# Kernel optimization log

Hardware: AMD Instinct MI355X
Metric: run time of the kernel (lower is better)

## Reference

```python
import jax, jax.numpy as jnp
import numpy as np

ATOM_FDIM, BOND_FDIM, HID, DEPTH = 133, 147, 256, 4
N_ATOMS, N_BONDS, MAX_NB, A_PER_MOL = 4096, 8192, 6, 64


def _ln(x, g, b, eps=1e-5):
    mu = x.mean(-1, keepdims=True)
    var = ((x - mu) ** 2).mean(-1, keepdims=True)
    return (x - mu) / jnp.sqrt(var + eps) * g + b


def setup_inputs() -> dict:
    key = jax.random.key(0)
    ks = jax.random.split(key, 20)
    def w(k, i, o):
        return jax.random.normal(k, (i, o), jnp.float32) / np.sqrt(i).astype(np.float32)
    return {
        "f_atoms": jax.random.normal(ks[0], (N_ATOMS, ATOM_FDIM), jnp.float32),
        "f_bonds": jax.random.normal(ks[1], (N_BONDS, BOND_FDIM), jnp.float32),
        "Wq_atom": w(ks[2], ATOM_FDIM, ATOM_FDIM),
        "Wk_atom": w(ks[3], ATOM_FDIM, ATOM_FDIM),
        "Wv_atom": w(ks[4], ATOM_FDIM, ATOM_FDIM),
        "ln_g": jnp.ones((ATOM_FDIM,), jnp.float32),
        "ln_b": jnp.zeros((ATOM_FDIM,), jnp.float32),
        "Wi": w(ks[5], BOND_FDIM, HID),
        "Wh": w(ks[6], HID, HID),
        "Wq": w(ks[7], HID, HID),
        "Wk": w(ks[8], HID, HID),
        "Wv": w(ks[9], HID, HID),
        "Wa": w(ks[10], HID, HID),
        "Walpha_w": w(ks[11], 2 * HID, 1),
        "Walpha_b": jnp.zeros((1,), jnp.float32),
        "Wo_w": w(ks[12], ATOM_FDIM + HID, HID),
        "Wo_b": jnp.zeros((HID,), jnp.float32),
        "Wb_w": w(ks[13], HID, HID),
        "Wb_b": jnp.zeros((HID,), jnp.float32),
        "a2b": jax.random.randint(ks[14], (N_ATOMS, MAX_NB), 0, N_BONDS),
        "b2a": jax.random.randint(ks[15], (N_BONDS,), 0, N_ATOMS),
        "b2revb": jax.random.randint(ks[16], (N_BONDS,), 0, N_BONDS),
        "atoms_per_mol": A_PER_MOL,
    }


def reference(f_atoms, f_bonds, Wq_atom, Wk_atom, Wv_atom, ln_g, ln_b, Wi, Wh,
              Wq, Wk, Wv, Wa, Walpha_w, Walpha_b, Wo_w, Wo_b, Wb_w, Wb_b,
              a2b, b2a, b2revb, atoms_per_mol):
    M = f_atoms.shape[0] // atoms_per_mol
    fdim = f_atoms.shape[1]
    # --- per-molecule atom self-attention enhancement (uniform a_scope) ---
    x = f_atoms.reshape(M, atoms_per_mol, fdim)  # [M, A, F]
    q, k, v = x @ Wq_atom, x @ Wk_atom, x @ Wv_atom
    scores = jnp.einsum('maf,mbf->mab', q, k) / np.sqrt(fdim).astype(np.float32)
    attn_out = jnp.einsum('mab,mbf->maf', jax.nn.softmax(scores, -1), v)
    f_atoms_e = _ln(x + attn_out, ln_g, ln_b).reshape(-1, fdim)

    # --- bond message init ---
    inputs = f_bonds @ Wi                      # [B, H]
    message = jax.nn.relu(inputs)
    sqrt_h = np.sqrt(HID).astype(np.float32)

    for _ in range(DEPTH - 1):
        # DMPNN gather-sum
        a_message = message[a2b].sum(1)        # [N_atoms, H]
        dmpnn = (a_message[b2a] - message[b2revb]) @ Wh
        # global bond-bond attention (faithful to torch: over all messages)
        Q, K, V = message @ Wq, message @ Wk, message @ Wv
        att_w = jax.nn.softmax(Q @ K.T / sqrt_h, -1)   # [B, B]
        att_msg = (att_w @ V) @ Wa
        alpha = jax.nn.sigmoid(
            jnp.concatenate([dmpnn, att_msg], -1) @ Walpha_w + Walpha_b)
        message = jax.nn.relu(inputs + alpha * dmpnn + (1.0 - alpha) * att_msg)
        # dropout is identity in eval mode

    # --- atom readout ---
    a_message = message[a2b].sum(1)
    a_input = jnp.concatenate([f_atoms_e, a_message], 1)
    atom_h = jax.nn.relu(a_input @ Wo_w + Wo_b)        # [N_atoms, H]

    # --- per-molecule attentive pooling ---
    hm = atom_h.reshape(M, atoms_per_mol, HID)
    aw = jax.nn.softmax(jnp.einsum('mah,mbh->mab', hm @ Wa, hm), -1)
    att_h = jax.nn.relu(jnp.einsum('mab,mbh->mah', aw, hm) @ Wb_w + Wb_b)
    mol_vecs = (hm + att_h).sum(1) / atoms_per_mol
    return mol_vecs
```

## Files before the change

kernel.cpp:

```cpp
#include <hip/hip_runtime.h>
#include <hip/hip_bf16.h>

typedef __hip_bfloat16 hbf16;
typedef __bf16 bf16x8 __attribute__((ext_vector_type(8)));
typedef float floatx4 __attribute__((ext_vector_type(4)));

#define N_ATOMS 4096
#define N_BONDS 8192
#define FDIM 133
#define BFDIM 147
#define HID 256
#define APM 64
#define NMOL 64
#define FA_S 160
#define FB_S 160
#define AI_S 416
#define CS 8

struct P8 { float* p[8]; };
struct QKV { const hbf16* w[3]; hbf16* outp[3]; };
struct CvtTab { const void* src[6]; float* dst[6]; int n[6]; };
struct WTab { const void* src[11]; hbf16* dst[11]; int K[11]; int Hout[11]; int Kp[11]; int total[11]; };

__device__ __forceinline__ float bcvt(hbf16 x) { return __bfloat162float(x); }

__device__ __forceinline__ float load_in(const void* src, int i, int f32flag)
{
    return f32flag ? ((const float*)src)[i] : bcvt(((const hbf16*)src)[i]);
}

__device__ __forceinline__ void split8(const float4 a0, const float4 a1,
                                       bf16x8& hi, bf16x8& lo)
{
    const float v[8] = {a0.x, a0.y, a0.z, a0.w, a1.x, a1.y, a1.z, a1.w};
    #pragma unroll
    for (int i = 0; i < 8; i++) {
        const __bf16 h = (__bf16)v[i];
        hi[i] = h;
        lo[i] = (__bf16)(v[i] - (float)h);
    }
}

__global__ void detect_kernel(const unsigned short* __restrict__ probe, int* __restrict__ flag)
{
    const int t = threadIdx.x;
    float mx = 0.f;
    for (int i = t; i < 4096; i += 64) {
        unsigned int u = ((unsigned int)probe[i]) << 16;
        float v;
        __builtin_memcpy(&v, &u, 4);
        v = fabsf(v);
        if (!(v == v)) v = 0.f;
        if (v > 1e6f) v = 1e6f;
        mx = fmaxf(mx, v);
    }
    #pragma unroll
    for (int o = 32; o > 0; o >>= 1) mx = fmaxf(mx, __shfl_xor(mx, o));
    if (t == 0) *flag = (mx > 100.f) ? 1 : 0;
}

__global__ void small_cvt_kernel(CvtTab tab, const int* __restrict__ flag)
{
    const int f32 = *flag;
    for (int s = 0; s < 6; s++)
        for (int i = threadIdx.x; i < tab.n[s]; i += 256)
            tab.dst[s][i] = load_in(tab.src[s], i, f32);
}

__global__ void cvt_pad_kernel(const void* __restrict__ src, float* __restrict__ dst,
                               int N, int K, int Kp, const int* __restrict__ flag)
{
    const int i = blockIdx.x * 256 + threadIdx.x;
    if (i >= N * Kp) return;
    const int r = i / Kp, k = i - r * Kp;
    dst[i] = (k < K) ? load_in(src, r * K + k, *flag) : 0.f;
}

__global__ void wt_all_kernel(WTab tab, const int* __restrict__ flag)
{
    const int wid = blockIdx.y;
    const int f32 = *flag;
    const int tot = tab.total[wid], Kp = tab.Kp[wid], K = tab.K[wid], Hout = tab.Hout[wid];
    hbf16* dst = tab.dst[wid];
    const void* src = tab.src[wid];
    for (int i = blockIdx.x * 256 + threadIdx.x; i < tot; i += gridDim.x * 256) {
        const int n = i / Kp, k = i - n * Kp;
        const float v = (k < K && n < Hout) ? load_in(src, k * Hout + n, f32) : 0.f;
        dst[i] = __float2bfloat16(v);
    }
}

__global__ __launch_bounds__(256)
void mgemm_kernel(const float* __restrict__ A, int lda, const hbf16* __restrict__ Wt,
                  const float* __restrict__ bias,
                  float* __restrict__ Cf, float* __restrict__ Cf2, int ldcf,
                  hbf16* __restrict__ Cbh, hbf16* __restrict__ Cbl, int ldcb,
                  hbf16* __restrict__ CbT, int ldct,
                  int Hout, int HoutStore, int relu)
{
    const int t = threadIdx.x, w = t >> 6, ln = t & 63;
    const int lane16 = ln & 15, quad = ln >> 4;
    const int rb = blockIdx.y * 64 + w * 16, cb = blockIdx.x * 64;
    const floatx4 zero4 = {0.f, 0.f, 0.f, 0.f};
    floatx4 acc[4] = {zero4, zero4, zero4, zero4};
    const float* ar = A + (size_t)(rb + lane16) * lda + quad * 8;
    for (int kk = 0; kk < lda; kk += 32) {
        const float4 a0 = *(const float4*)(ar + kk);
        const float4 a1 = *(const float4*)(ar + kk + 4);
        bf16x8 af;
        af[0] = (__bf16)a0.x; af[1] = (__bf16)a0.y; af[2] = (__bf16)a0.z; af[3] = (__bf16)a0.w;
        af[4] = (__bf16)a1.x; af[5] = (__bf16)a1.y; af[6] = (__bf16)a1.z; af[7] = (__bf16)a1.w;
        #pragma unroll
        for (int nt = 0; nt < 4; nt++) {
            const bf16x8 bf =
                *(const bf16x8*)&Wt[(size_t)(cb + nt * 16 + lane16) * lda + kk + quad * 8];
            acc[nt] = __builtin_amdgcn_mfma_f32_16x16x32_bf16(af, bf, acc[nt], 0, 0, 0);
        }
    }
    #pragma unroll
    for (int nt = 0; nt < 4; nt++) {
        const int n = cb + nt * 16 + lane16;
        if (n >= HoutStore) continue;
        const bool valid = n < Hout;
        const float bv = (bias && valid) ? bias[n] : 0.f;
        #pragma unroll
        for (int r = 0; r < 4; r++) {
            const int m = rb + quad * 4 + r;
            float v = valid ? acc[nt][r] + bv : 0.f;
            if (relu) v = fmaxf(v, 0.f);
            if (Cf)  Cf[(size_t)m * ldcf + n] = v;
            if (Cf2) Cf2[(size_t)m * ldcf + n] = fmaxf(v, 0.f);
            if (Cbh) {
                const hbf16 h = __float2bfloat16(v);
                Cbh[(size_t)m * ldcb + n] = h;
                if (Cbl) Cbl[(size_t)m * ldcb + n] = __float2bfloat16(v - bcvt(h));
            }
            if (CbT) CbT[(size_t)n * ldct + m] = __float2bfloat16(v);
        }
    }
}

__global__ __launch_bounds__(256)
void qkv_kernel(const float* __restrict__ A, QKV q)
{
    const int z = blockIdx.z;
    const hbf16* __restrict__ Wt = q.w[z];
    hbf16* __restrict__ outp = q.outp[z];
    const int t = threadIdx.x, w = t >> 6, ln = t & 63;
    const int lane16 = ln & 15, quad = ln >> 4;
    const int rb = blockIdx.y * 64 + w * 16, cb = blockIdx.x * 64;
    const floatx4 zero4 = {0.f, 0.f, 0.f, 0.f};
    floatx4 acc[4] = {zero4, zero4, zero4, zero4};
    const float* ar = A + (size_t)(rb + lane16) * HID + quad * 8;
    for (int kk = 0; kk < HID; kk += 32) {
        const float4 a0 = *(const float4*)(ar + kk);
        const float4 a1 = *(const float4*)(ar + kk + 4);
        bf16x8 af;
        af[0] = (__bf16)a0.x; af[1] = (__bf16)a0.y; af[2] = (__bf16)a0.z; af[3] = (__bf16)a0.w;
        af[4] = (__bf16)a1.x; af[5] = (__bf16)a1.y; af[6] = (__bf16)a1.z; af[7] = (__bf16)a1.w;
        #pragma unroll
        for (int nt = 0; nt < 4; nt++) {
            const bf16x8 bf =
                *(const bf16x8*)&Wt[(size_t)(cb + nt * 16 + lane16) * HID + kk + quad * 8];
            acc[nt] = __builtin_amdgcn_mfma_f32_16x16x32_bf16(af, bf, acc[nt], 0, 0, 0);
        }
    }
    #pragma unroll
    for (int nt = 0; nt < 4; nt++) {
        const int n = cb + nt * 16 + lane16;
        #pragma unroll
        for (int r = 0; r < 4; r++) {
            const int m = rb + quad * 4 + r;
            const hbf16 h = __float2bfloat16(acc[nt][r]);
            if (z < 2) outp[(size_t)m * HID + n] = h;
            else       outp[(size_t)n * N_BONDS + m] = h;
        }
    }
}

__global__ __launch_bounds__(256)
void atom_fused_kernel(const float* __restrict__ qa, const float* __restrict__ ka,
                       const hbf16* __restrict__ vT, const float* __restrict__ f_atoms_p,
                       const float* __restrict__ ln_g, const float* __restrict__ ln_b,
                       float* __restrict__ f_e)
{
    __shared__ float S[64][68];
    __shared__ __bf16 P[64][72];
    __shared__ float Y[64][136];
    const int m = blockIdx.x, t = threadIdx.x;
    const int w = t >> 6, ln = t & 63;
    const int lane16 = ln & 15, quad = ln >> 4;
    const int base = m * APM;
    const floatx4 zero4 = {0.f, 0.f, 0.f, 0.f};

    {
        floatx4 acc[4] = {zero4, zero4, zero4, zero4};
        const float* arow = qa + (size_t)(base + w * 16 + lane16) * FA_S + quad * 8;
        #pragma unroll
        for (int ks = 0; ks < 5; ks++) {
            bf16x8 ah, al;
            split8(*(const float4*)(arow + ks * 32), *(const float4*)(arow + ks * 32 + 4), ah, al);
            #pragma unroll
            for (int nt = 0; nt < 4; nt++) {
                const float* brow = ka + (size_t)(base + nt * 16 + lane16) * FA_S + ks * 32 + quad * 8;
                bf16x8 bh, bl;
                split8(*(const float4*)brow, *(const float4*)(brow + 4), bh, bl);
                acc[nt] = __builtin_amdgcn_mfma_f32_16x16x32_bf16(ah, bh, acc[nt], 0, 0, 0);
                acc[nt] = __builtin_amdgcn_mfma_f32_16x16x32_bf16(al, bh, acc[nt], 0, 0, 0);
                acc[nt] = __builtin_amdgcn_mfma_f32_16x16x32_bf16(ah, bl, acc[nt], 0, 0, 0);
            }
        }
        const float scale = 1.f / sqrtf(133.f);
        #pragma unroll
        for (int nt = 0; nt < 4; nt++)
            #pragma unroll
            for (int r = 0; r < 4; r++)
                S[w * 16 + quad * 4 + r][nt * 16 + lane16] = acc[nt][r] * scale;
    }
    for (int r = w * 16; r < w * 16 + 16; r++) {
        const float x = S[r][ln];
        float mx = x;
        #pragma unroll
        for (int o = 32; o > 0; o >>= 1) mx = fmaxf(mx, __shfl_xor(mx, o));
        const float p = __expf(x - mx);
        float sm = p;
        #pragma unroll
        for (int o = 32; o > 0; o >>= 1) sm += __shfl_xor(sm, o);
        P[r][ln] = (__bf16)(p / sm);
    }
    {
        floatx4 o[9];
        #pragma unroll
        for (int i = 0; i < 9; i++) o[i] = zero4;
        #pragma unroll
        for (int ks = 0; ks < 2; ks++) {
            const bf16x8 af = *(const bf16x8*)&P[w * 16 + lane16][ks * 32 + quad * 8];
            #pragma unroll
            for (int nt = 0; nt < 9; nt++) {
                const bf16x8 bfv =
                    *(const bf16x8*)&vT[(size_t)(nt * 16 + lane16) * N_ATOMS + base + ks * 32 + quad * 8];
                o[nt] = __builtin_amdgcn_mfma_f32_16x16x32_bf16(af, bfv, o[nt], 0, 0, 0);
            }
        }
        #pragma unroll
        for (int nt = 0; nt < 9; nt++) {
            const int f = nt * 16 + lane16;
            if (f >= FDIM) continue;
            #pragma unroll
            for (int r = 0; r < 4; r++) {
                const int a = w * 16 + quad * 4 + r;
                Y[a][f] = f_atoms_p[(size_t)(base + a) * FA_S + f] + o[nt][r];
            }
        }
    }
    for (int r = w * 16; r < w * 16 + 16; r++) {
        float sum = 0.f, sq = 0.f;
        for (int f = ln; f < FDIM; f += 64) { const float v = Y[r][f]; sum += v; sq += v * v; }
        #pragma unroll
        for (int o = 32; o > 0; o >>= 1) { sum += __shfl_xor(sum, o); sq += __shfl_xor(sq, o); }
        const float mu = sum / FDIM;
        const float var = sq / FDIM - mu * mu;
        const float rstd = rsqrtf(var + 1e-5f);
        for (int f = ln; f < FDIM; f += 64) {
            const float v = (Y[r][f] - mu) * rstd;
            f_e[(size_t)(base + r) * FDIM + f] = v * ln_g[f] + ln_b[f];
        }
    }
}

__global__ __launch_bounds__(256)
void pool_fused_kernel(const float* __restrict__ hmWa, const float* __restrict__ atom_h,
                       const hbf16* __restrict__ hm_hi, const hbf16* __restrict__ hm_lo,
                       const hbf16* __restrict__ hmT, const hbf16* __restrict__ Wtb,
                       const float* __restrict__ Wb_b, void* __restrict__ out,
                       const int* __restrict__ flag)
{
    __shared__ float S[64][68];
    __shared__ __bf16 P[64][72];
    __shared__ __bf16 att[64][264];
    const int m = blockIdx.x, t = threadIdx.x;
    const int w = t >> 6, ln = t & 63;
    const int lane16 = ln & 15, quad = ln >> 4;
    const int base = m * APM;
    const floatx4 zero4 = {0.f, 0.f, 0.f, 0.f};

    {
        floatx4 acc[4] = {zero4, zero4, zero4, zero4};
        const float* arow = hmWa + (size_t)(base + w * 16 + lane16) * HID + quad * 8;
        #pragma unroll
        for (int ks = 0; ks < 8; ks++) {
            bf16x8 ah, al;
            split8(*(const float4*)(arow + ks * 32), *(const float4*)(arow + ks * 32 + 4), ah, al);
            #pragma unroll
            for (int nt = 0; nt < 4; nt++) {
                const size_t bidx = (size_t)(base + nt * 16 + lane16) * HID + ks * 32 + quad * 8;
                const bf16x8 bh = *(const bf16x8*)&hm_hi[bidx];
                const bf16x8 bl = *(const bf16x8*)&hm_lo[bidx];
                acc[nt] = __builtin_amdgcn_mfma_f32_16x16x32_bf16(ah, bh, acc[nt], 0, 0, 0);
                acc[nt] = __builtin_amdgcn_mfma_f32_16x16x32_bf16(al, bh, acc[nt], 0, 0, 0);
                acc[nt] = __builtin_amdgcn_mfma_f32_16x16x32_bf16(ah, bl, acc[nt], 0, 0, 0);
            }
        }
        #pragma unroll
        for (int nt = 0; nt < 4; nt++)
            #pragma unroll
            for (int r = 0; r < 4; r++)
                S[w * 16 + quad * 4 + r][nt * 16 + lane16] = acc[nt][r];
    }
    for (int r = w * 16; r < w * 16 + 16; r++) {
        const float x = S[r][ln];
        float mx = x;
        #pragma unroll
        for (int o = 32; o > 0; o >>= 1) mx = fmaxf(mx, __shfl_xor(mx, o));
        const float p = __expf(x - mx);
        float sm = p;
        #pragma unroll
        for (int o = 32; o > 0; o >>= 1) sm += __shfl_xor(sm, o);
        P[r][ln] = (__bf16)(p / sm);
    }
    __syncthreads();
    {
        floatx4 o3[4][4];
        #pragma unroll
        for (int mt = 0; mt < 4; mt++)
            #pragma unroll
            for (int nt = 0; nt < 4; nt++) o3[mt][nt] = zero4;
        #pragma unroll
        for (int ks = 0; ks < 2; ks++) {
            bf16x8 af[4];
            #pragma unroll
            for (int mt = 0; mt < 4; mt++)
                af[mt] = *(const bf16x8*)&P[mt * 16 + lane16][ks * 32 + quad * 8];
            #pragma unroll
            for (int nt = 0; nt < 4; nt++) {
                const bf16x8 bfv = *(const bf16x8*)
                    &hmT[(size_t)(w * 64 + nt * 16 + lane16) * N_ATOMS + base + ks * 32 + quad * 8];
                #pragma unroll
                for (int mt = 0; mt < 4; mt++)
                    o3[mt][nt] = __builtin_amdgcn_mfma_f32_16x16x32_bf16(af[mt], bfv, o3[mt][nt], 0, 0, 0);
            }
        }
        #pragma unroll
        for (int mt = 0; mt < 4; mt++)
            #pragma unroll
            for (int nt = 0; nt < 4; nt++)
                #pragma unroll
                for (int r = 0; r < 4; r++)
                    att[mt * 16 + quad * 4 + r][w * 64 + nt * 16 + lane16] = (__bf16)o3[mt][nt][r];
    }
    __syncthreads();
    {
        floatx4 o5[4][4];
        #pragma unroll
        for (int mt = 0; mt < 4; mt++)
            #pragma unroll
            for (int nt = 0; nt < 4; nt++) o5[mt][nt] = zero4;
        #pragma unroll
        for (int ks = 0; ks < 8; ks++) {
            bf16x8 af[4];
            #pragma unroll
            for (int mt = 0; mt < 4; mt++)
                af[mt] = *(const bf16x8*)&att[mt * 16 + lane16][ks * 32 + quad * 8];
            #pragma unroll
            for (int nt = 0; nt < 4; nt++) {
                const bf16x8 bfv = *(const bf16x8*)
                    &Wtb[(size_t)(w * 64 + nt * 16 + lane16) * HID + ks * 32 + quad * 8];
                #pragma unroll
                for (int mt = 0; mt < 4; mt++)
                    o5[mt][nt] = __builtin_amdgcn_mfma_f32_16x16x32_bf16(af[mt], bfv, o5[mt][nt], 0, 0, 0);
            }
        }
        #pragma unroll
        for (int nt = 0; nt < 4; nt++) {
            const int n = w * 64 + nt * 16 + lane16;
            const float bv = Wb_b[n];
            float s = 0.f;
            #pragma unroll
            for (int mt = 0; mt < 4; mt++)
                #pragma unroll
                for (int r = 0; r < 4; r++)
                    s += fmaxf(o5[mt][nt][r] + bv, 0.f);
            s += __shfl_xor(s, 16);
            s += __shfl_xor(s, 32);
            if (quad == 0) {
                float hsum = 0.f;
                for (int a = 0; a < APM; a++)
                    hsum += atom_h[(size_t)(base + a) * HID + n];
                const float v = (s + hsum) * (1.f / 64.f);
                if (*flag) ((float*)out)[m * HID + n] = v;
                else       ((hbf16*)out)[m * HID + n] = __float2bfloat16(v);
            }
        }
    }
}

__global__ __launch_bounds__(256, 2)
void flash_kernel(const hbf16* __restrict__ Qg, const hbf16* __restrict__ Kg,
                  const hbf16* __restrict__ Vtg, P8 parts, float2* __restrict__ ml)
{
    __shared__ __align__(16) __bf16 Ks[32][256];
    __shared__ __align__(16) __bf16 Vt[256][32];
    __shared__ __align__(16) __bf16 Ps[4][16][40];

    const int t = threadIdx.x, w = t >> 6, ln = t & 63;
    const int lane16 = ln & 15, quad = ln >> 4;
    const int cs = blockIdx.x;
    const int rw = blockIdx.y * 64 + w * 16;
    float* __restrict__ part = parts.p[cs];

    bf16x8 qf[8];
    #pragma unroll
    for (int ks = 0; ks < 8; ks++)
        qf[ks] = *(const bf16x8*)&Qg[(size_t)(rw + lane16) * HID + ks * 32 + quad * 8];

    const floatx4 zero4 = {0.f, 0.f, 0.f, 0.f};
    floatx4 O[16];
    #pragma unroll
    for (int i = 0; i < 16; i++) O[i] = zero4;
    float mrow[4] = {-1e30f, -1e30f, -1e30f, -1e30f};
    float lrow[4] = {0.f, 0.f, 0.f, 0.f};
    const float scale = 0.0625f;

    const int cbeg = cs * (N_BONDS / CS), cend = cbeg + N_BONDS / CS;
    for (int c0 = cbeg; c0 < cend; c0 += 32) {
        __syncthreads();
        #pragma unroll
        for (int ii = 0; ii < 4; ii++) {
            const int idx = t + ii * 256;
            const int row = idx >> 5, c = idx & 31;
            *(bf16x8*)&Ks[row][(c ^ (row & 31)) * 8] =
                *(const bf16x8*)&Kg[(size_t)(c0 + row) * HID + c * 8];
        }
        #pragma unroll
        for (int ii = 0; ii < 4; ii++) {
            const int idx = t + ii * 256;
            const int row = idx >> 2, c = idx & 3;
            *(bf16x8*)&Vt[row][(c ^ (row & 3)) * 8] =
                *(const bf16x8*)&Vtg[(size_t)row * N_BONDS + c0 + c * 8];
        }
        __syncthreads();

        floatx4 s0 = zero4, s1 = zero4;
        #pragma unroll
        for (int ks = 0; ks < 8; ks++) {
            const int ch = ks * 4 + quad;
            const bf16x8 b0 = *(bf16x8*)&Ks[lane16][(ch ^ lane16) * 8];
            const bf16x8 b1 = *(bf16x8*)&Ks[16 + lane16][(ch ^ (16 + lane16)) * 8];
            s0 = __builtin_amdgcn_mfma_f32_16x16x32_bf16(qf[ks], b0, s0, 0, 0, 0);
            s1 = __builtin_amdgcn_mfma_f32_16x16x32_bf16(qf[ks], b1, s1, 0, 0, 0);
        }
        float alpha[4];
        #pragma unroll
        for (int r = 0; r < 4; r++) {
            const float v0 = s0[r] * scale, v1 = s1[r] * scale;
            float mx = fmaxf(v0, v1);
            #pragma unroll
            for (int o = 8; o > 0; o >>= 1) mx = fmaxf(mx, __shfl_xor(mx, o));
            const float mnew = fmaxf(mrow[r], mx);
            const float p0 = __expf(v0 - mnew), p1 = __expf(v1 - mnew);
            float ps = p0 + p1;
            #pragma unroll
            for (int o = 8; o > 0; o >>= 1) ps += __shfl_xor(ps, o);
            alpha[r] = __expf(mrow[r] - mnew);
            lrow[r] = lrow[r] * alpha[r] + ps;
            mrow[r] = mnew;
            const int row = quad * 4 + r;
            Ps[w][row][lane16] = (__bf16)p0;
            Ps[w][row][16 + lane16] = (__bf16)p1;
        }
        const bool need = (alpha[0] < 1.f) | (alpha[1] < 1.f) | (alpha[2] < 1.f) | (alpha[3] < 1.f);
        if (__any(need)) {
            #pragma unroll
            for (int nt = 0; nt < 16; nt++)
                #pragma unroll
                for (int r = 0; r < 4; r++) O[nt][r] *= alpha[r];
        }
        const bf16x8 pf = *(bf16x8*)&Ps[w][lane16][quad * 8];
        #pragma unroll
        for (int nt = 0; nt < 16; nt++) {
            const int vrow = nt * 16 + lane16;
            const bf16x8 vf = *(bf16x8*)&Vt[vrow][(quad ^ (vrow & 3)) * 8];
            O[nt] = __builtin_amdgcn_mfma_f32_16x16x32_bf16(pf, vf, O[nt], 0, 0, 0);
        }
    }
    #pragma unroll
    for (int r = 0; r < 4; r++) {
        const int row = rw + quad * 4 + r;
        #pragma unroll
        for (int nt = 0; nt < 16; nt++)
            part[(size_t)row * HID + nt * 16 + lane16] = O[nt][r];
        if (lane16 == 0) ml[cs * N_BONDS + row] = make_float2(mrow[r], lrow[r]);
    }
}

__global__ void flash_combine_kernel(P8 parts, const float2* __restrict__ ml,
                                     float* __restrict__ out)
{
    const int row = blockIdx.x, h = threadIdx.x;
    float2 e[CS];
    float M = -1e30f;
    #pragma unroll
    for (int i = 0; i < CS; i++) { e[i] = ml[i * N_BONDS + row]; M = fmaxf(M, e[i].x); }
    float den = 0.f, val = 0.f;
    #pragma unroll
    for (int i = 0; i < CS; i++) {
        const float wgt = __expf(e[i].x - M);
        den += wgt * e[i].y;
        val += wgt * parts.p[i][(size_t)row * HID + h];
    }
    out[(size_t)row * HID + h] = val / den;
}

__global__ void gather_kernel(const float* __restrict__ msg, const int* __restrict__ a2b,
                              float* __restrict__ amsg)
{
    const int a = blockIdx.x, h = threadIdx.x;
    float s = 0.f;
    #pragma unroll
    for (int i = 0; i < 6; i++) {
        const int b = a2b[a * 6 + i];
        s += msg[(size_t)b * HID + h];
    }
    amsg[(size_t)a * HID + h] = s;
}

__global__ void pre_kernel(const float* __restrict__ amsg, const float* __restrict__ msg,
                           const int* __restrict__ b2a, const int* __restrict__ b2revb,
                           float* __restrict__ pre)
{
    const int b = blockIdx.x, h = threadIdx.x;
    pre[(size_t)b * HID + h] =
        amsg[(size_t)b2a[b] * HID + h] - msg[(size_t)b2revb[b] * HID + h];
}

__global__ __launch_bounds__(256)
void combine_kernel(const float* __restrict__ inputs, const float* __restrict__ dmpnn,
                    const float* __restrict__ att, const float* __restrict__ ww,
                    const float* __restrict__ wb, float* __restrict__ msg)
{
    const int wv = threadIdx.x >> 6, lnid = threadIdx.x & 63;
    const int row = blockIdx.x * 4 + wv;
    const float* dr = dmpnn + (size_t)row * HID;
    const float* ar = att + (size_t)row * HID;
    float dot = 0.f;
    for (int h = lnid; h < HID; h += 64)
        dot += dr[h] * ww[h] + ar[h] * ww[HID + h];
    #pragma unroll
    for (int o = 32; o > 0; o >>= 1) dot += __shfl_xor(dot, o);
    const float alpha = 1.f / (1.f + __expf(-(dot + wb[0])));
    for (int h = lnid; h < HID; h += 64) {
        const float v = inputs[(size_t)row * HID + h] + alpha * dr[h] + (1.f - alpha) * ar[h];
        msg[(size_t)row * HID + h] = fmaxf(v, 0.f);
    }
}

__global__ void concat_kernel(const float* __restrict__ fe, const float* __restrict__ amsg,
                              float* __restrict__ ai)
{
    const int a = blockIdx.x, t = threadIdx.x;
    for (int f = t; f < FDIM; f += 256) ai[(size_t)a * AI_S + f] = fe[(size_t)a * FDIM + f];
    for (int h = t; h < HID; h += 256) ai[(size_t)a * AI_S + FDIM + h] = amsg[(size_t)a * HID + h];
    for (int z = t; z < AI_S - FDIM - HID; z += 256) ai[(size_t)a * AI_S + FDIM + HID + z] = 0.f;
}

extern "C" void kernel_launch(void* const* d_in, const int* in_sizes, int n_in,
                              void* d_out, int out_size, void* d_ws, size_t ws_size,
                              hipStream_t stream)
{
    const int* a2b    = (const int*)d_in[19];
    const int* b2a    = (const int*)d_in[20];
    const int* b2revb = (const int*)d_in[21];

    float* ws = (float*)d_ws;
    size_t off = 0;
    auto alloc = [&](size_t n) { float* p = ws + off; off += (n + 63) & ~(size_t)63; return p; };
    int* flag = (int*)alloc(64);

    float* ln_g     = alloc(FDIM);
    float* ln_b     = alloc(FDIM);
    float* Walpha_w = alloc(2 * HID);
    float* Walpha_b = alloc(64);
    float* Wo_b     = alloc(HID);
    float* Wb_b     = alloc(HID);
    float* f_atoms_p = alloc((size_t)N_ATOMS * FA_S);
    float* f_bonds_p = alloc((size_t)N_BONDS * FB_S);
    auto balloc = [&](size_t n) { return (hbf16*)alloc((n + 1) / 2); };
    hbf16* Wt_qa = balloc((size_t)192 * FA_S);
    hbf16* Wt_ka = balloc((size_t)192 * FA_S);
    hbf16* Wt_va = balloc((size_t)192 * FA_S);
    hbf16* Wt_i  = balloc((size_t)HID * FB_S);
    hbf16* Wt_h  = balloc((size_t)HID * HID);
    hbf16* Wt_q  = balloc((size_t)HID * HID);
    hbf16* Wt_k  = balloc((size_t)HID * HID);
    hbf16* Wt_v  = balloc((size_t)HID * HID);
    hbf16* Wt_a  = balloc((size_t)HID * HID);
    hbf16* Wt_b  = balloc((size_t)HID * HID);
    hbf16* Wt_o  = balloc((size_t)HID * AI_S);

    float* f_e    = alloc((size_t)N_ATOMS * FDIM);
    float* inputs = alloc((size_t)N_BONDS * HID);
    float* msg    = alloc((size_t)N_BONDS * HID);
    float* buf1   = alloc((size_t)N_BONDS * HID);
    float* buf2   = alloc((size_t)N_BONDS * HID);
    float* buf3   = alloc((size_t)N_BONDS * HID);
    float* buf4   = alloc((size_t)N_BONDS * HID);
    float* pnew   = alloc((size_t)N_BONDS * HID);
    float* pext0  = alloc((size_t)N_BONDS * HID);
    float* pext1  = alloc((size_t)N_BONDS * HID);
    float* pext2  = alloc((size_t)N_BONDS * HID);
    float* pext3  = alloc((size_t)N_BONDS * HID);
    float* amsg   = alloc((size_t)N_ATOMS * HID);
    float2* ml    = (float2*)alloc((size_t)CS * N_BONDS * 2);
    hbf16* Qb  = balloc((size_t)N_BONDS * HID);
    hbf16* Kb  = balloc((size_t)N_BONDS * HID);
    hbf16* Vtg = balloc((size_t)N_BONDS * HID);
    hbf16* vTa = (hbf16*)buf3;

    detect_kernel<<<1, 64, 0, stream>>>((const unsigned short*)d_in[1], flag);

    CvtTab ct;
    ct.src[0] = d_in[5];  ct.dst[0] = ln_g;     ct.n[0] = FDIM;
    ct.src[1] = d_in[6];  ct.dst[1] = ln_b;     ct.n[1] = FDIM;
    ct.src[2] = d_in[13]; ct.dst[2] = Walpha_w; ct.n[2] = 2 * HID;
    ct.src[3] = d_in[14]; ct.dst[3] = Walpha_b; ct.n[3] = 1;
    ct.src[4] = d_in[16]; ct.dst[4] = Wo_b;     ct.n[4] = HID;
    ct.src[5] = d_in[18]; ct.dst[5] = Wb_b;     ct.n[5] = HID;
    small_cvt_kernel<<<1, 256, 0, stream>>>(ct, flag);

    cvt_pad_kernel<<<(N_ATOMS * FA_S + 255) / 256, 256, 0, stream>>>(
        d_in[0], f_atoms_p, N_ATOMS, FDIM, FA_S, flag);
    cvt_pad_kernel<<<(N_BONDS * FB_S + 255) / 256, 256, 0, stream>>>(
        d_in[1], f_bonds_p, N_BONDS, BFDIM, FB_S, flag);

    WTab wt;
    const void* wsrc[11] = {d_in[2], d_in[3], d_in[4], d_in[7], d_in[8], d_in[9],
                            d_in[10], d_in[11], d_in[12], d_in[17], d_in[15]};
    hbf16* wdst[11] = {Wt_qa, Wt_ka, Wt_va, Wt_i, Wt_h, Wt_q, Wt_k, Wt_v, Wt_a, Wt_b, Wt_o};
    const int wK[11]  = {FDIM, FDIM, FDIM, BFDIM, HID, HID, HID, HID, HID, HID, FDIM + HID};
    const int wH[11]  = {FDIM, FDIM, FDIM, HID, HID, HID, HID, HID, HID, HID, HID};
    const int wKp[11] = {FA_S, FA_S, FA_S, FB_S, HID, HID, HID, HID, HID, HID, AI_S};
    const int wHp[11] = {192, 192, 192, HID, HID, HID, HID, HID, HID, HID, HID};
    for (int i = 0; i < 11; i++) {
        wt.src[i] = wsrc[i]; wt.dst[i] = wdst[i]; wt.K[i] = wK[i]; wt.Hout[i] = wH[i];
        wt.Kp[i] = wKp[i]; wt.total[i] = wHp[i] * wKp[i];
    }
    wt_all_kernel<<<dim3(416, 11), 256, 0, stream>>>(wt, flag);

    auto mg = [&](const float* A, int lda, const hbf16* Wt, const float* bias,
                  float* Cf, float* Cf2, int ldcf, hbf16* Cbh, hbf16* Cbl, int ldcb,
                  hbf16* CbT, int ldct, int rows, int Hout, int HoutStore, int relu) {
        dim3 grid((HoutStore + 63) / 64, rows / 64);
        mgemm_kernel<<<grid, 256, 0, stream>>>(A, lda, Wt, bias, Cf, Cf2, ldcf,
                                               Cbh, Cbl, ldcb, CbT, ldct,
                                               Hout, HoutStore, relu);
    };

    mg(f_atoms_p, FA_S, Wt_qa, nullptr, buf1, nullptr, FA_S, nullptr, nullptr, 0,
       nullptr, 0, N_ATOMS, FDIM, FA_S, 0);
    mg(f_atoms_p, FA_S, Wt_ka, nullptr, buf2, nullptr, FA_S, nullptr, nullptr, 0,
       nullptr, 0, N_ATOMS, FDIM, FA_S, 0);
    mg(f_atoms_p, FA_S, Wt_va, nullptr, nullptr, nullptr, 0, nullptr, nullptr, 0,
       vTa, N_ATOMS, N_ATOMS, FDIM, 192, 0);
    atom_fused_kernel<<<NMOL, 256, 0, stream>>>(buf1, buf2, vTa, f_atoms_p, ln_g, ln_b, f_e);

    mg(f_bonds_p, FB_S, Wt_i, nullptr, inputs, msg, HID, nullptr, nullptr, 0,
       nullptr, 0, N_BONDS, HID, HID, 0);

    P8 parts;
    parts.p[0] = buf1; parts.p[1] = buf3; parts.p[2] = buf4; parts.p[3] = pnew;
    parts.p[4] = pext0; parts.p[5] = pext1; parts.p[6] = pext2; parts.p[7] = pext3;
    QKV qkv;
    qkv.w[0] = Wt_q; qkv.w[1] = Wt_k; qkv.w[2] = Wt_v;
    qkv.outp[0] = Qb; qkv.outp[1] = Kb; qkv.outp[2] = Vtg;

    for (int d = 0; d < 3; d++) {
        gather_kernel<<<N_ATOMS, 256, 0, stream>>>(msg, a2b, amsg);
        pre_kernel<<<N_BONDS, 256, 0, stream>>>(amsg, msg, b2a, b2revb, buf1);
        mg(buf1, HID, Wt_h, nullptr, buf2, nullptr, HID, nullptr, nullptr, 0,
           nullptr, 0, N_BONDS, HID, HID, 0);
        qkv_kernel<<<dim3(4, N_BONDS / 64, 3), 256, 0, stream>>>(msg, qkv);
        flash_kernel<<<dim3(CS, N_BONDS / 64), 256, 0, stream>>>(Qb, Kb, Vtg, parts, ml);
        flash_combine_kernel<<<N_BONDS, 256, 0, stream>>>(parts, ml, buf3);
        mg(buf3, HID, Wt_a, nullptr, buf4, nullptr, HID, nullptr, nullptr, 0,
           nullptr, 0, N_BONDS, HID, HID, 0);
        combine_kernel<<<N_BONDS / 4, 256, 0, stream>>>(inputs, buf2, buf4, Walpha_w,
                                                        Walpha_b, msg);
    }

    gather_kernel<<<N_ATOMS, 256, 0, stream>>>(msg, a2b, amsg);
    concat_kernel<<<N_ATOMS, 256, 0, stream>>>(f_e, amsg, buf1);
    mg(buf1, AI_S, Wt_o, Wo_b, buf4, nullptr, HID, Qb, Kb, HID,
       Vtg, N_ATOMS, N_ATOMS, HID, HID, 1);

    mg(buf4, HID, Wt_a, nullptr, buf3, nullptr, HID, nullptr, nullptr, 0,
       nullptr, 0, N_ATOMS, HID, HID, 0);
    pool_fused_kernel<<<NMOL, 256, 0, stream>>>(buf3, buf4, Qb, Kb, Vtg, Wt_b,
                                                Wb_b, d_out, flag);
}
```

Baseline: 1.061 ms.

## Fuse flash split combine with Wa GEMM and gating; double rows per flash wave

Each flash-attention wave now processes 32 query rows instead of 16, so every K/V tile loaded into shared memory feeds twice as many MFMAs. The split-KV combine, the Wa projection and the alpha-gated relu update are merged into one kernel that rebuilds the attention output in LDS as bf16 and writes msg directly. The atom gather and the bond pre-subtraction are also merged into a single kernel. This removes several launches and intermediate global round trips, at the cost of higher register pressure in the flash kernel, half as many flash blocks, and a bf16 rounding of the attention output before Wa.

```diff
diff --git a/kernel.cpp b/kernel.cpp
--- a/kernel.cpp
+++ b/kernel.cpp
@@ -400,25 +400,32 @@
 {
     __shared__ __align__(16) __bf16 Ks[32][256];
     __shared__ __align__(16) __bf16 Vt[256][32];
-    __shared__ __align__(16) __bf16 Ps[4][16][40];
+    __shared__ __align__(16) __bf16 Ps[4][32][40];
 
     const int t = threadIdx.x, w = t >> 6, ln = t & 63;
     const int lane16 = ln & 15, quad = ln >> 4;
     const int cs = blockIdx.x;
-    const int rw = blockIdx.y * 64 + w * 16;
+    const int rw = blockIdx.y * 128 + w * 32;
     float* __restrict__ part = parts.p[cs];
 
-    bf16x8 qf[8];
-    #pragma unroll
-    for (int ks = 0; ks < 8; ks++)
-        qf[ks] = *(const bf16x8*)&Qg[(size_t)(rw + lane16) * HID + ks * 32 + quad * 8];
+    bf16x8 qf[2][8];
+    #pragma unroll
+    for (int mt = 0; mt < 2; mt++)
+        #pragma unroll
+        for (int ks = 0; ks < 8; ks++)
+            qf[mt][ks] = *(const bf16x8*)&Qg[(size_t)(rw + mt * 16 + lane16) * HID + ks * 32 + quad * 8];
 
     const floatx4 zero4 = {0.f, 0.f, 0.f, 0.f};
-    floatx4 O[16];
-    #pragma unroll
-    for (int i = 0; i < 16; i++) O[i] = zero4;
-    float mrow[4] = {-1e30f, -1e30f, -1e30f, -1e30f};
-    float lrow[4] = {0.f, 0.f, 0.f, 0.f};
+    floatx4 O[2][16];
+    #pragma unroll
+    for (int mt = 0; mt < 2; mt++)
+        #pragma unroll
+        for (int i = 0; i < 16; i++) O[mt][i] = zero4;
+    float mrow[2][4], lrow[2][4];
+    #pragma unroll
+    for (int mt = 0; mt < 2; mt++)
+        #pragma unroll
+        for (int r = 0; r < 4; r++) { mrow[mt][r] = -1e30f; lrow[mt][r] = 0.f; }
     const float scale = 0.0625f;
 
     const int cbeg = cs * (N_BONDS / CS), cend = cbeg + N_BONDS / CS;
@@ -440,75 +447,157 @@
         }
         __syncthreads();
 
-        floatx4 s0 = zero4, s1 = zero4;
+        floatx4 s[2][2] = {{zero4, zero4}, {zero4, zero4}};
         #pragma unroll
         for (int ks = 0; ks < 8; ks++) {
             const int ch = ks * 4 + quad;
             const bf16x8 b0 = *(bf16x8*)&Ks[lane16][(ch ^ lane16) * 8];
             const bf16x8 b1 = *(bf16x8*)&Ks[16 + lane16][(ch ^ (16 + lane16)) * 8];
-            s0 = __builtin_amdgcn_mfma_f32_16x16x32_bf16(qf[ks], b0, s0, 0, 0, 0);
-            s1 = __builtin_amdgcn_mfma_f32_16x16x32_bf16(qf[ks], b1, s1, 0, 0, 0);
-        }
-        float alpha[4];
-        #pragma unroll
-        for (int r = 0; r < 4; r++) {
-            const float v0 = s0[r] * scale, v1 = s1[r] * scale;
-            float mx = fmaxf(v0, v1);
-            #pragma unroll
-            for (int o = 8; o > 0; o >>= 1) mx = fmaxf(mx, __shfl_xor(mx, o));
-            const float mnew = fmaxf(mrow[r], mx);
-            const float p0 = __expf(v0 - mnew), p1 = __expf(v1 - mnew);
-            float ps = p0 + p1;
-            #pragma unroll
-            for (int o = 8; o > 0; o >>= 1) ps += __shfl_xor(ps, o);
-            alpha[r] = __expf(mrow[r] - mnew);
-            lrow[r] = lrow[r] * alpha[r] + ps;
-            mrow[r] = mnew;
-            const int row = quad * 4 + r;
-            Ps[w][row][lane16] = (__bf16)p0;
-            Ps[w][row][16 + lane16] = (__bf16)p1;
-        }
-        const bool need = (alpha[0] < 1.f) | (alpha[1] < 1.f) | (alpha[2] < 1.f) | (alpha[3] < 1.f);
+            #pragma unroll
+            for (int mt = 0; mt < 2; mt++) {
+                s[mt][0] = __builtin_amdgcn_mfma_f32_16x16x32_bf16(qf[mt][ks], b0, s[mt][0], 0, 0, 0);
+                s[mt][1] = __builtin_amdgcn_mfma_f32_16x16x32_bf16(qf[mt][ks], b1, s[mt][1], 0, 0, 0);
+            }
+        }
+        float alpha[2][4];
+        bool need = false;
+        #pragma unroll
+        for (int mt = 0; mt < 2; mt++)
+            #pragma unroll
+            for (int r = 0; r < 4; r++) {
+                const float v0 = s[mt][0][r] * scale, v1 = s[mt][1][r] * scale;
+                float mx = fmaxf(v0, v1);
+                #pragma unroll
+                for (int o = 8; o > 0; o >>= 1) mx = fmaxf(mx, __shfl_xor(mx, o));
+                const float mnew = fmaxf(mrow[mt][r], mx);
+                const float p0 = __expf(v0 - mnew), p1 = __expf(v1 - mnew);
+                float ps = p0 + p1;
+                #pragma unroll
+                for (int o = 8; o > 0; o >>= 1) ps += __shfl_xor(ps, o);
+                alpha[mt][r] = __expf(mrow[mt][r] - mnew);
+                need |= (alpha[mt][r] < 1.f);
+                lrow[mt][r] = lrow[mt][r] * alpha[mt][r] + ps;
+                mrow[mt][r] = mnew;
+                const int row = mt * 16 + quad * 4 + r;
+                Ps[w][row][lane16] = (__bf16)p0;
+                Ps[w][row][16 + lane16] = (__bf16)p1;
+            }
         if (__any(need)) {
             #pragma unroll
-            for (int nt = 0; nt < 16; nt++)
+            for (int mt = 0; mt < 2; mt++)
                 #pragma unroll
-                for (int r = 0; r < 4; r++) O[nt][r] *= alpha[r];
-        }
-        const bf16x8 pf = *(bf16x8*)&Ps[w][lane16][quad * 8];
+                for (int nt = 0; nt < 16; nt++)
+                    #pragma unroll
+                    for (int r = 0; r < 4; r++) O[mt][nt][r] *= alpha[mt][r];
+        }
+        bf16x8 pf[2];
+        #pragma unroll
+        for (int mt = 0; mt < 2; mt++)
+            pf[mt] = *(bf16x8*)&Ps[w][mt * 16 + lane16][quad * 8];
         #pragma unroll
         for (int nt = 0; nt < 16; nt++) {
             const int vrow = nt * 16 + lane16;
             const bf16x8 vf = *(bf16x8*)&Vt[vrow][(quad ^ (vrow & 3)) * 8];
-            O[nt] = __builtin_amdgcn_mfma_f32_16x16x32_bf16(pf, vf, O[nt], 0, 0, 0);
-        }
-    }
+            #pragma unroll
+            for (int mt = 0; mt < 2; mt++)
+                O[mt][nt] = __builtin_amdgcn_mfma_f32_16x16x32_bf16(pf[mt], vf, O[mt][nt], 0, 0, 0);
+        }
+    }
+    #pragma unroll
+    for (int mt = 0; mt < 2; mt++)
+        #pragma unroll
+        for (int r = 0; r < 4; r++) {
+            const int row = rw + mt * 16 + quad * 4 + r;
+            #pragma unroll
+            for (int nt = 0; nt < 16; nt++)
+                part[(size_t)row * HID + nt * 16 + lane16] = O[mt][nt][r];
+            if (lane16 == 0) ml[cs * N_BONDS + row] = make_float2(mrow[mt][r], lrow[mt][r]);
+        }
+}
+
+__global__ __launch_bounds__(256)
+void attcombine_kernel(P8 parts, const float2* __restrict__ ml, const hbf16* __restrict__ Wta,
+                       const float* __restrict__ inputs, const float* __restrict__ dmpnn,
+                       const float* __restrict__ ww, const float* __restrict__ wb,
+                       float* __restrict__ msg)
+{
+    __shared__ __align__(16) __bf16 Av[64][264];
+    __shared__ float wgtS[64][10];
+    const int t = threadIdx.x, w = t >> 6, ln = t & 63;
+    const int lane16 = ln & 15, quad = ln >> 4;
+    const int rb = blockIdx.x * 64;
+
+    if (t < 64) {
+        const int row = rb + t;
+        float2 e[CS];
+        float M = -1e30f;
+        #pragma unroll
+        for (int i = 0; i < CS; i++) { e[i] = ml[i * N_BONDS + row]; M = fmaxf(M, e[i].x); }
+        float den = 0.f;
+        #pragma unroll
+        for (int i = 0; i < CS; i++) {
+            const float g = __expf(e[i].x - M);
+            wgtS[t][i] = g;
+            den += g * e[i].y;
+        }
+        wgtS[t][8] = 1.f / den;
+    }
+    __syncthreads();
+    for (int e = t; e < 64 * 64; e += 256) {
+        const int row = e >> 6, c4 = (e & 63) * 4;
+        const float inv = wgtS[row][8];
+        float ax = 0.f, ay = 0.f, az = 0.f, aw = 0.f;
+        #pragma unroll
+        for (int i = 0; i < CS; i++) {
+            const float g = wgtS[row][i];
+            const float4 pv = *(const float4*)&parts.p[i][(size_t)(rb + row) * HID + c4];
+            ax += g * pv.x; ay += g * pv.y; az += g * pv.z; aw += g * pv.w;
+        }
+        Av[row][c4 + 0] = (__bf16)(ax * inv);
+        Av[row][c4 + 1] = (__bf16)(ay * inv);
+        Av[row][c4 + 2] = (__bf16)(az * inv);
+        Av[row][c4 + 3] = (__bf16)(aw * inv);
+    }
+    __syncthreads();
+
+    const floatx4 zero4 = {0.f, 0.f, 0.f, 0.f};
+    floatx4 acc[16];
+    #pragma unroll
+    for (int nt = 0; nt < 16; nt++) acc[nt] = zero4;
+    #pragma unroll
+    for (int ks = 0; ks < 8; ks++) {
+        const bf16x8 af = *(const bf16x8*)&Av[w * 16 + lane16][ks * 32 + quad * 8];
+        #pragma unroll
+        for (int nt = 0; nt < 16; nt++) {
+            const bf16x8 bf = *(const bf16x8*)&Wta[(size_t)(nt * 16 + lane16) * HID + ks * 32 + quad * 8];
+            acc[nt] = __builtin_amdgcn_mfma_f32_16x16x32_bf16(af, bf, acc[nt], 0, 0, 0);
+        }
+    }
+    float w2[16];
+    #pragma unroll
+    for (int nt = 0; nt < 16; nt++) w2[nt] = ww[HID + nt * 16 + lane16];
     #pragma unroll
     for (int r = 0; r < 4; r++) {
-        const int row = rw + quad * 4 + r;
-        #pragma unroll
-        for (int nt = 0; nt < 16; nt++)
-            part[(size_t)row * HID + nt * 16 + lane16] = O[nt][r];
-        if (lane16 == 0) ml[cs * N_BONDS + row] = make_float2(mrow[r], lrow[r]);
-    }
-}
-
-__global__ void flash_combine_kernel(P8 parts, const float2* __restrict__ ml,
-                                     float* __restrict__ out)
-{
-    const int row = blockIdx.x, h = threadIdx.x;
-    float2 e[CS];
-    float M = -1e30f;
-    #pragma unroll
-    for (int i = 0; i < CS; i++) { e[i] = ml[i * N_BONDS + row]; M = fmaxf(M, e[i].x); }
-    float den = 0.f, val = 0.f;
-    #pragma unroll
-    for (int i = 0; i < CS; i++) {
-        const float wgt = __expf(e[i].x - M);
-        den += wgt * e[i].y;
-        val += wgt * parts.p[i][(size_t)row * HID + h];
-    }
-    out[(size_t)row * HID + h] = val / den;
+        const int row = rb + w * 16 + quad * 4 + r;
+        float dv[16], iv[16];
+        float dot = 0.f;
+        #pragma unroll
+        for (int nt = 0; nt < 16; nt++) {
+            const int col = nt * 16 + lane16;
+            dv[nt] = dmpnn[(size_t)row * HID + col];
+            iv[nt] = inputs[(size_t)row * HID + col];
+            dot += acc[nt][r] * w2[nt] + dv[nt] * ww[col];
+        }
+        #pragma unroll
+        for (int o = 8; o > 0; o >>= 1) dot += __shfl_xor(dot, o);
+        const float alpha = 1.f / (1.f + __expf(-(dot + wb[0])));
+        #pragma unroll
+        for (int nt = 0; nt < 16; nt++) {
+            const int col = nt * 16 + lane16;
+            const float v = iv[nt] + alpha * dv[nt] + (1.f - alpha) * acc[nt][r];
+            msg[(size_t)row * HID + col] = fmaxf(v, 0.f);
+        }
+    }
 }
 
 __global__ void gather_kernel(const float* __restrict__ msg, const int* __restrict__ a2b,
@@ -524,34 +613,17 @@
     amsg[(size_t)a * HID + h] = s;
 }
 
-__global__ void pre_kernel(const float* __restrict__ amsg, const float* __restrict__ msg,
-                           const int* __restrict__ b2a, const int* __restrict__ b2revb,
-                           float* __restrict__ pre)
+__global__ void gather_pre_kernel(const float* __restrict__ msg, const int* __restrict__ a2b,
+                                  const int* __restrict__ b2a, const int* __restrict__ b2revb,
+                                  float* __restrict__ pre)
 {
     const int b = blockIdx.x, h = threadIdx.x;
-    pre[(size_t)b * HID + h] =
-        amsg[(size_t)b2a[b] * HID + h] - msg[(size_t)b2revb[b] * HID + h];
-}
-
-__global__ __launch_bounds__(256)
-void combine_kernel(const float* __restrict__ inputs, const float* __restrict__ dmpnn,
-                    const float* __restrict__ att, const float* __restrict__ ww,
-                    const float* __restrict__ wb, float* __restrict__ msg)
-{
-    const int wv = threadIdx.x >> 6, lnid = threadIdx.x & 63;
-    const int row = blockIdx.x * 4 + wv;
-    const float* dr = dmpnn + (size_t)row * HID;
-    const float* ar = att + (size_t)row * HID;
-    float dot = 0.f;
-    for (int h = lnid; h < HID; h += 64)
-        dot += dr[h] * ww[h] + ar[h] * ww[HID + h];
-    #pragma unroll
-    for (int o = 32; o > 0; o >>= 1) dot += __shfl_xor(dot, o);
-    const float alpha = 1.f / (1.f + __expf(-(dot + wb[0])));
-    for (int h = lnid; h < HID; h += 64) {
-        const float v = inputs[(size_t)row * HID + h] + alpha * dr[h] + (1.f - alpha) * ar[h];
-        msg[(size_t)row * HID + h] = fmaxf(v, 0.f);
-    }
+    const int a = b2a[b];
+    float s = -msg[(size_t)b2revb[b] * HID + h];
+    #pragma unroll
+    for (int i = 0; i < 6; i++)
+        s += msg[(size_t)a2b[a * 6 + i] * HID + h];
+    pre[(size_t)b * HID + h] = s;
 }
 
 __global__ void concat_kernel(const float* __restrict__ fe, const float* __restrict__ amsg,
@@ -674,17 +746,13 @@
     qkv.outp[0] = Qb; qkv.outp[1] = Kb; qkv.outp[2] = Vtg;
 
     for (int d = 0; d < 3; d++) {
-        gather_kernel<<<N_ATOMS, 256, 0, stream>>>(msg, a2b, amsg);
-        pre_kernel<<<N_BONDS, 256, 0, stream>>>(amsg, msg, b2a, b2revb, buf1);
+        gather_pre_kernel<<<N_BONDS, 256, 0, stream>>>(msg, a2b, b2a, b2revb, buf1);
         mg(buf1, HID, Wt_h, nullptr, buf2, nullptr, HID, nullptr, nullptr, 0,
            nullptr, 0, N_BONDS, HID, HID, 0);
         qkv_kernel<<<dim3(4, N_BONDS / 64, 3), 256, 0, stream>>>(msg, qkv);
-        flash_kernel<<<dim3(CS, N_BONDS / 64), 256, 0, stream>>>(Qb, Kb, Vtg, parts, ml);
-        flash_combine_kernel<<<N_BONDS, 256, 0, stream>>>(parts, ml, buf3);
-        mg(buf3, HID, Wt_a, nullptr, buf4, nullptr, HID, nullptr, nullptr, 0,
-           nullptr, 0, N_BONDS, HID, HID, 0);
-        combine_kernel<<<N_BONDS / 4, 256, 0, stream>>>(inputs, buf2, buf4, Walpha_w,
-                                                        Walpha_b, msg);
+        flash_kernel<<<dim3(CS, N_BONDS / 128), 256, 0, stream>>>(Qb, Kb, Vtg, parts, ml);
+        attcombine_kernel<<<N_BONDS / 64, 256, 0, stream>>>(parts, ml, Wt_a, inputs,
+                                                            buf2, Walpha_w, Walpha_b, msg);
     }
 
     gather_kernel<<<N_ATOMS, 256, 0, stream>>>(msg, a2b, amsg);
```

Result: slower. 1.236 ms (+16.5%).

## Fuse depth-loop kernels: gather+pre, Wh into QKV launch, flash-combine+Wa+gating

Applied to the files above, without the earlier changes.

Merges the atom gather and bond pre-subtraction into one kernel and folds the Wh projection into the batched Q/K/V projection launch. The flash partial combine, Wa projection, alpha gate and ReLU update now run in a single kernel per 32-row tile. This cuts launches and round trips of intermediate bond-sized buffers through global memory. It also changes the flash kernel occupancy hint to 3 waves per EU. The Wh and Wa projections now use single bf16 inputs instead of the previous generic GEMM path, which may reduce accuracy.

```diff
diff --git a/kernel.cpp b/kernel.cpp
--- a/kernel.cpp
+++ b/kernel.cpp
@@ -18,7 +18,7 @@
 #define CS 8
 
 struct P8 { float* p[8]; };
-struct QKV { const hbf16* w[3]; hbf16* outp[3]; };
+struct PROJ { const float* A[4]; const hbf16* w[4]; void* outp[4]; int mode[4]; };
 struct CvtTab { const void* src[6]; float* dst[6]; int n[6]; };
 struct WTab { const void* src[11]; hbf16* dst[11]; int K[11]; int Hout[11]; int Kp[11]; int total[11]; };
 
@@ -141,11 +141,13 @@
 }
 
 __global__ __launch_bounds__(256)
-void qkv_kernel(const float* __restrict__ A, QKV q)
+void proj_kernel(PROJ p)
 {
     const int z = blockIdx.z;
-    const hbf16* __restrict__ Wt = q.w[z];
-    hbf16* __restrict__ outp = q.outp[z];
+    const float* __restrict__ A = p.A[z];
+    const hbf16* __restrict__ Wt = p.w[z];
+    void* __restrict__ outp = p.outp[z];
+    const int mode = p.mode[z];
     const int t = threadIdx.x, w = t >> 6, ln = t & 63;
     const int lane16 = ln & 15, quad = ln >> 4;
     const int rb = blockIdx.y * 64 + w * 16, cb = blockIdx.x * 64;
@@ -171,9 +173,10 @@
         #pragma unroll
         for (int r = 0; r < 4; r++) {
             const int m = rb + quad * 4 + r;
-            const hbf16 h = __float2bfloat16(acc[nt][r]);
-            if (z < 2) outp[(size_t)m * HID + n] = h;
-            else       outp[(size_t)n * N_BONDS + m] = h;
+            const float v = acc[nt][r];
+            if (mode == 2)      ((float*)outp)[(size_t)m * HID + n] = v;
+            else if (mode == 0) ((hbf16*)outp)[(size_t)m * HID + n] = __float2bfloat16(v);
+            else                ((hbf16*)outp)[(size_t)n * N_BONDS + m] = __float2bfloat16(v);
         }
     }
 }
@@ -394,7 +397,7 @@
     }
 }
 
-__global__ __launch_bounds__(256, 2)
+__global__ __launch_bounds__(256) __attribute__((amdgpu_waves_per_eu(3, 3)))
 void flash_kernel(const hbf16* __restrict__ Qg, const hbf16* __restrict__ Kg,
                   const hbf16* __restrict__ Vtg, P8 parts, float2* __restrict__ ml)
 {
@@ -493,22 +496,96 @@
     }
 }
 
-__global__ void flash_combine_kernel(P8 parts, const float2* __restrict__ ml,
-                                     float* __restrict__ out)
-{
-    const int row = blockIdx.x, h = threadIdx.x;
-    float2 e[CS];
-    float M = -1e30f;
-    #pragma unroll
-    for (int i = 0; i < CS; i++) { e[i] = ml[i * N_BONDS + row]; M = fmaxf(M, e[i].x); }
-    float den = 0.f, val = 0.f;
-    #pragma unroll
-    for (int i = 0; i < CS; i++) {
-        const float wgt = __expf(e[i].x - M);
-        den += wgt * e[i].y;
-        val += wgt * parts.p[i][(size_t)row * HID + h];
-    }
-    out[(size_t)row * HID + h] = val / den;
+__global__ __launch_bounds__(256)
+void attcombine_kernel(P8 parts, const float2* __restrict__ ml, const hbf16* __restrict__ Wta,
+                       const float* __restrict__ inputs, const float* __restrict__ dmpnn,
+                       const float* __restrict__ ww, const float* __restrict__ wb,
+                       float* __restrict__ msg)
+{
+    __shared__ __align__(16) __bf16 Av[32][264];
+    __shared__ float wgtS[32][10];
+    __shared__ float dotS[32][2];
+    const int t = threadIdx.x, w = t >> 6, ln = t & 63;
+    const int lane16 = ln & 15, quad = ln >> 4;
+    const int rb = blockIdx.x * 32;
+    const int mt = w & 1, nh = w >> 1;
+
+    if (t < 32) {
+        const int row = rb + t;
+        float2 e[CS];
+        float M = -1e30f;
+        #pragma unroll
+        for (int i = 0; i < CS; i++) { e[i] = ml[i * N_BONDS + row]; M = fmaxf(M, e[i].x); }
+        float den = 0.f;
+        #pragma unroll
+        for (int i = 0; i < CS; i++) {
+            const float g = __expf(e[i].x - M);
+            wgtS[t][i] = g;
+            den += g * e[i].y;
+        }
+        wgtS[t][8] = 1.f / den;
+    }
+    __syncthreads();
+    for (int e = t; e < 32 * 64; e += 256) {
+        const int row = e >> 6, c4 = (e & 63) * 4;
+        const float inv = wgtS[row][8];
+        float ax = 0.f, ay = 0.f, az = 0.f, aw = 0.f;
+        #pragma unroll
+        for (int i = 0; i < CS; i++) {
+            const float g = wgtS[row][i];
+            const float4 pv = *(const float4*)&parts.p[i][(size_t)(rb + row) * HID + c4];
+            ax += g * pv.x; ay += g * pv.y; az += g * pv.z; aw += g * pv.w;
+        }
+        Av[row][c4 + 0] = (__bf16)(ax * inv);
+        Av[row][c4 + 1] = (__bf16)(ay * inv);
+        Av[row][c4 + 2] = (__bf16)(az * inv);
+        Av[row][c4 + 3] = (__bf16)(aw * inv);
+    }
+    __syncthreads();
+
+    const floatx4 zero4 = {0.f, 0.f, 0.f, 0.f};
+    floatx4 acc[8];
+    #pragma unroll
+    for (int nt = 0; nt < 8; nt++) acc[nt] = zero4;
+    #pragma unroll
+    for (int ks = 0; ks < 8; ks++) {
+        const bf16x8 af = *(const bf16x8*)&Av[mt * 16 + lane16][ks * 32 + quad * 8];
+        #pragma unroll
+        for (int nt = 0; nt < 8; nt++) {
+            const bf16x8 bf = *(const bf16x8*)
+                &Wta[(size_t)(nh * 128 + nt * 16 + lane16) * HID + ks * 32 + quad * 8];
+            acc[nt] = __builtin_amdgcn_mfma_f32_16x16x32_bf16(af, bf, acc[nt], 0, 0, 0);
+        }
+    }
+    float w2[8];
+    #pragma unroll
+    for (int nt = 0; nt < 8; nt++) w2[nt] = ww[HID + nh * 128 + nt * 16 + lane16];
+    #pragma unroll
+    for (int r = 0; r < 4; r++) {
+        const int row = rb + mt * 16 + quad * 4 + r;
+        float dot = 0.f;
+        #pragma unroll
+        for (int nt = 0; nt < 8; nt++) {
+            const int col = nh * 128 + nt * 16 + lane16;
+            dot += acc[nt][r] * w2[nt] + dmpnn[(size_t)row * HID + col] * ww[col];
+        }
+        #pragma unroll
+        for (int o = 8; o > 0; o >>= 1) dot += __shfl_xor(dot, o);
+        if (lane16 == 0) dotS[row - rb][nh] = dot;
+    }
+    __syncthreads();
+    #pragma unroll
+    for (int r = 0; r < 4; r++) {
+        const int row = rb + mt * 16 + quad * 4 + r;
+        const float alpha = 1.f / (1.f + __expf(-(dotS[row - rb][0] + dotS[row - rb][1] + wb[0])));
+        #pragma unroll
+        for (int nt = 0; nt < 8; nt++) {
+            const int col = nh * 128 + nt * 16 + lane16;
+            const float dv = dmpnn[(size_t)row * HID + col];
+            const float v = inputs[(size_t)row * HID + col] + alpha * dv + (1.f - alpha) * acc[nt][r];
+            msg[(size_t)row * HID + col] = fmaxf(v, 0.f);
+        }
+    }
 }
 
 __global__ void gather_kernel(const float* __restrict__ msg, const int* __restrict__ a2b,
@@ -524,34 +601,17 @@
     amsg[(size_t)a * HID + h] = s;
 }
 
-__global__ void pre_kernel(const float* __restrict__ amsg, const float* __restrict__ msg,
-                           const int* __restrict__ b2a, const int* __restrict__ b2revb,
-                           float* __restrict__ pre)
+__global__ void gather_pre_kernel(const float* __restrict__ msg, const int* __restrict__ a2b,
+                                  const int* __restrict__ b2a, const int* __restrict__ b2revb,
+                                  float* __restrict__ pre)
 {
     const int b = blockIdx.x, h = threadIdx.x;
-    pre[(size_t)b * HID + h] =
-        amsg[(size_t)b2a[b] * HID + h] - msg[(size_t)b2revb[b] * HID + h];
-}
-
-__global__ __launch_bounds__(256)
-void combine_kernel(const float* __restrict__ inputs, const float* __restrict__ dmpnn,
-                    const float* __restrict__ att, const float* __restrict__ ww,
-                    const float* __restrict__ wb, float* __restrict__ msg)
-{
-    const int wv = threadIdx.x >> 6, lnid = threadIdx.x & 63;
-    const int row = blockIdx.x * 4 + wv;
-    const float* dr = dmpnn + (size_t)row * HID;
-    const float* ar = att + (size_t)row * HID;
-    float dot = 0.f;
-    for (int h = lnid; h < HID; h += 64)
-        dot += dr[h] * ww[h] + ar[h] * ww[HID + h];
-    #pragma unroll
-    for (int o = 32; o > 0; o >>= 1) dot += __shfl_xor(dot, o);
-    const float alpha = 1.f / (1.f + __expf(-(dot + wb[0])));
-    for (int h = lnid; h < HID; h += 64) {
-        const float v = inputs[(size_t)row * HID + h] + alpha * dr[h] + (1.f - alpha) * ar[h];
-        msg[(size_t)row * HID + h] = fmaxf(v, 0.f);
-    }
+    const int a = b2a[b];
+    float s = -msg[(size_t)b2revb[b] * HID + h];
+    #pragma unroll
+    for (int i = 0; i < 6; i++)
+        s += msg[(size_t)a2b[a * 6 + i] * HID + h];
+    pre[(size_t)b * HID + h] = s;
 }
 
 __global__ void concat_kernel(const float* __restrict__ fe, const float* __restrict__ amsg,
@@ -669,22 +729,18 @@
     P8 parts;
     parts.p[0] = buf1; parts.p[1] = buf3; parts.p[2] = buf4; parts.p[3] = pnew;
     parts.p[4] = pext0; parts.p[5] = pext1; parts.p[6] = pext2; parts.p[7] = pext3;
-    QKV qkv;
-    qkv.w[0] = Wt_q; qkv.w[1] = Wt_k; qkv.w[2] = Wt_v;
-    qkv.outp[0] = Qb; qkv.outp[1] = Kb; qkv.outp[2] = Vtg;
+    PROJ pj;
+    pj.A[0] = buf1; pj.w[0] = Wt_h; pj.outp[0] = buf2; pj.mode[0] = 2;
+    pj.A[1] = msg;  pj.w[1] = Wt_q; pj.outp[1] = Qb;   pj.mode[1] = 0;
+    pj.A[2] = msg;  pj.w[2] = Wt_k; pj.outp[2] = Kb;   pj.mode[2] = 0;
+    pj.A[3] = msg;  pj.w[3] = Wt_v; pj.outp[3] = Vtg;  pj.mode[3] = 1;
 
     for (int d = 0; d < 3; d++) {
-        gather_kernel<<<N_ATOMS, 256, 0, stream>>>(msg, a2b, amsg);
-        pre_kernel<<<N_BONDS, 256, 0, stream>>>(amsg, msg, b2a, b2revb, buf1);
-        mg(buf1, HID, Wt_h, nullptr, buf2, nullptr, HID, nullptr, nullptr, 0,
-           nullptr, 0, N_BONDS, HID, HID, 0);
-        qkv_kernel<<<dim3(4, N_BONDS / 64, 3), 256, 0, stream>>>(msg, qkv);
+        gather_pre_kernel<<<N_BONDS, 256, 0, stream>>>(msg, a2b, b2a, b2revb, buf1);
+        proj_kernel<<<dim3(4, N_BONDS / 64, 4), 256, 0, stream>>>(pj);
         flash_kernel<<<dim3(CS, N_BONDS / 64), 256, 0, stream>>>(Qb, Kb, Vtg, parts, ml);
-        flash_combine_kernel<<<N_BONDS, 256, 0, stream>>>(parts, ml, buf3);
-        mg(buf3, HID, Wt_a, nullptr, buf4, nullptr, HID, nullptr, nullptr, 0,
-           nullptr, 0, N_BONDS, HID, HID, 0);
-        combine_kernel<<<N_BONDS / 4, 256, 0, stream>>>(inputs, buf2, buf4, Walpha_w,
-                                                        Walpha_b, msg);
+        attcombine_kernel<<<N_BONDS / 32, 256, 0, stream>>>(parts, ml, Wt_a, inputs,
+                                                            buf2, Walpha_w, Walpha_b, msg);
     }
 
     gather_kernel<<<N_ATOMS, 256, 0, stream>>>(msg, a2b, amsg);
```

Result: slower. 1.268 ms (+19.5%).
